# Optimization experiments

Measured on AMD Instinct MI355X. Metric: run time of the kernel, lower is better.

The kernel has to match this reference:

```python
import jax, jax.numpy as jnp
import numpy as np

NUM_EMBEDDINGS = 8192
EMBEDDING_DIM = 256
COMMITMENT_COST = 0.25


def setup_inputs() -> dict:
    key = jax.random.key(0)
    k1, k2 = jax.random.split(key)
    x = jax.random.normal(k1, (8, 4096, EMBEDDING_DIM), dtype=jnp.float32)
    # torch init: uniform(-1/K, 1/K)
    codebook = jax.random.uniform(
        k2, (NUM_EMBEDDINGS, EMBEDDING_DIM), dtype=jnp.float32,
        minval=-1.0 / NUM_EMBEDDINGS, maxval=1.0 / NUM_EMBEDDINGS)
    return {"x": x, "codebook": codebook}


def reference(x, codebook):
    D = codebook.shape[1]
    K = codebook.shape[0]
    flat_x = x.reshape(-1, D)                      # [N, D]
    distances = (jnp.sum(flat_x * flat_x, axis=1, keepdims=True)
                 + jnp.sum(codebook * codebook, axis=1)
                 - 2.0 * jnp.matmul(flat_x, codebook.T))
    encoding_indices = jnp.argmin(distances, axis=1)  # [N]
    # direct gather instead of one-hot matmul (same math)
    quantized = codebook[encoding_indices].reshape(x.shape)

    sg = jax.lax.stop_gradient
    e_latent_loss = jnp.mean((sg(quantized) - x) ** 2)
    q_latent_loss = jnp.mean((quantized - sg(x)) ** 2)
    loss = q_latent_loss + COMMITMENT_COST * e_latent_loss

    quantized_st = x + sg(quantized - x)

    # avg one-hot probs via counts
    counts = jnp.bincount(encoding_indices, length=K)
    avg_probs = counts.astype(x.dtype) / encoding_indices.shape[0]
    perplexity = jnp.exp(-jnp.sum(avg_probs * jnp.log(avg_probs + 1e-10)))
    return quantized_st, loss, perplexity
```

## Files before the change

kernel.cpp:

```cpp
#include <hip/hip_runtime.h>
#include <cfloat>
#include <math.h>

#define NUM_EMB 8192
#define DIM 256
#define NROWS 32768
#define NSPLIT 4
#define CHUNKS 32

typedef float f32x4 __attribute__((ext_vector_type(4)));
typedef int   i32x4 __attribute__((ext_vector_type(4)));
typedef int   i32x8 __attribute__((ext_vector_type(8)));

#define GL2LDS(g, l) __builtin_amdgcn_global_load_lds( \
    (const __attribute__((address_space(1))) void*)(g), \
    (__attribute__((address_space(3))) void*)(l), 16, 0, 0)

#define MFMA(A, B, C) __builtin_amdgcn_mfma_scale_f32_16x16x128_f8f6f4( \
    (A), (B), (C), 0, 0, 0, 127, 0, 127)

__global__ __launch_bounds__(256) void vq_prep(const float* __restrict__ x,
                                               unsigned char* __restrict__ xq,
                                               const float* __restrict__ cb,
                                               unsigned char* __restrict__ cbq,
                                               float* __restrict__ cbn,
                                               unsigned int* __restrict__ counts) {
    int b = blockIdx.x;
    if (b < 4096) {
        int i = b * 256 + threadIdx.x;
        float4 v0 = ((const float4*)x)[2 * i];
        float4 v1 = ((const float4*)x)[2 * i + 1];
        int p0 = __builtin_amdgcn_cvt_pk_fp8_f32(-v0.x, -v0.y, 0, false);
        p0     = __builtin_amdgcn_cvt_pk_fp8_f32(-v0.z, -v0.w, p0, true);
        int p1 = __builtin_amdgcn_cvt_pk_fp8_f32(-v1.x, -v1.y, 0, false);
        p1     = __builtin_amdgcn_cvt_pk_fp8_f32(-v1.z, -v1.w, p1, true);
        ((int2*)xq)[i] = make_int2(p0, p1);
    } else if (b < 6144) {
        int row  = (b - 4096) * 4 + (threadIdx.x >> 6);
        int lane = threadIdx.x & 63;
        float4 v = ((const float4*)(cb + (size_t)row * DIM))[lane];
        int p = __builtin_amdgcn_cvt_pk_fp8_f32(v.x * 8192.f, v.y * 8192.f, 0, false);
        p     = __builtin_amdgcn_cvt_pk_fp8_f32(v.z * 8192.f, v.w * 8192.f, p, true);
        ((int*)cbq)[row * 64 + lane] = p;
        float s = v.x * v.x + v.y * v.y + v.z * v.z + v.w * v.w;
        #pragma unroll
        for (int off = 32; off > 0; off >>= 1) s += __shfl_down(s, off, 64);
        if (lane == 0) cbn[row] = 4096.f * s + 256.f;
    } else {
        counts[(b - 6144) * 256 + threadIdx.x] = 0u;
    }
}

__global__ __launch_bounds__(256, 4) void vq_argmin_mfma(
        const unsigned char* __restrict__ xq,
        const unsigned char* __restrict__ cbq,
        const float* __restrict__ cbn,
        unsigned long long* __restrict__ partial) {
    __shared__ __align__(16) unsigned char Bs[2][16384];
    __shared__ unsigned long long redk[2][64];

    const int tid = threadIdx.x;
    const int lane = tid & 63;
    const int w = tid >> 6;
    const int wm = w >> 1, wn = w & 1;
    const int l15 = lane & 15, q = lane >> 4;
    const int ns = blockIdx.x & (NSPLIT - 1);
    const int by = blockIdx.x >> 2;
    const int m0 = by * 64;
    const int nbase = ns * (NUM_EMB / NSPLIT);

    i32x8 afr00, afr01, afr10, afr11;
    {
        const unsigned char* p = xq + (size_t)(m0 + wm * 32 + l15) * 256 + q * 32;
        i32x4 lo, hi;
        lo = *(const i32x4*)(p);                  hi = *(const i32x4*)(p + 16);
        afr00 = __builtin_shufflevector(lo, hi, 0, 1, 2, 3, 4, 5, 6, 7);
        lo = *(const i32x4*)(p + 16 * 256);       hi = *(const i32x4*)(p + 16 * 256 + 16);
        afr01 = __builtin_shufflevector(lo, hi, 0, 1, 2, 3, 4, 5, 6, 7);
        lo = *(const i32x4*)(p + 128);            hi = *(const i32x4*)(p + 128 + 16);
        afr10 = __builtin_shufflevector(lo, hi, 0, 1, 2, 3, 4, 5, 6, 7);
        lo = *(const i32x4*)(p + 16 * 256 + 128); hi = *(const i32x4*)(p + 16 * 256 + 128 + 16);
        afr11 = __builtin_shufflevector(lo, hi, 0, 1, 2, 3, 4, 5, 6, 7);
    }

    const int row0 = wn * 32 + l15;
    const int sw = row0 & 7;
    const int vA = row0 * 256 + (((2 * q) ^ sw) * 16);
    const int vB = row0 * 256 + (((2 * q + 1) ^ sw) * 16);

    const unsigned int colb0 = (unsigned)(wn * 32 + l15);
    const unsigned int colb1 = colb0 + 16;

    unsigned int runk[2][4];
    #pragma unroll
    for (int i = 0; i < 2; i++)
        #pragma unroll
        for (int r = 0; r < 4; r++) runk[i][r] = 0xFFFFFFFFu;

    const int sr = lane >> 4;
    const int sv = lane & 15;
    const int kcs = sv >> 3, blk = sv & 7;
    const unsigned char* gs[4];
    int sg[4];
    #pragma unroll
    for (int t = 0; t < 4; t++) {
        int s = t * 4 + w;
        int r = s * 4 + sr;
        gs[t] = cbq + (size_t)(nbase + r) * 256 + (size_t)(kcs * 128 + ((blk ^ (r & 7)) * 16));
        sg[t] = s * 1024;
    }

    #pragma unroll
    for (int t = 0; t < 4; t++) GL2LDS(gs[t], (char*)&Bs[0][0] + sg[t]);
    #pragma unroll
    for (int t = 0; t < 4; t++) gs[t] += 16384;
    const float* bnp = cbn + nbase;
    float bn0 = bnp[colb0];
    float bn1 = bnp[colb1];
    __syncthreads();

#define BLOAD(CUR, OFF) ({ \
    i32x4 lo_ = *(const i32x4*)(&Bs[CUR][0] + vA + (OFF)); \
    i32x4 hi_ = *(const i32x4*)(&Bs[CUR][0] + vB + (OFF)); \
    __builtin_shufflevector(lo_, hi_, 0, 1, 2, 3, 4, 5, 6, 7); })

#define CHUNK_BODY(CHV, CUR, NXT, LAST) do { \
    float nbn0 = bnp[64 + (int)colb0]; \
    float nbn1 = bnp[64 + (int)colb1]; \
    if (!(LAST)) { \
        GL2LDS(gs[0], (char*)&Bs[NXT][0] + sg[0]); \
        GL2LDS(gs[1], (char*)&Bs[NXT][0] + sg[1]); \
        GL2LDS(gs[2], (char*)&Bs[NXT][0] + sg[2]); \
        GL2LDS(gs[3], (char*)&Bs[NXT][0] + sg[3]); \
    } \
    gs[0] += 16384; gs[1] += 16384; gs[2] += 16384; gs[3] += 16384; \
    f32x4 ci0; ci0[0] = bn0; ci0[1] = bn0; ci0[2] = bn0; ci0[3] = bn0; \
    f32x4 ci1; ci1[0] = bn1; ci1[1] = bn1; ci1[2] = bn1; ci1[3] = bn1; \
    i32x8 b_ = BLOAD(CUR, 0); \
    f32x4 a00 = MFMA(afr00, b_, ci0); \
    f32x4 a10 = MFMA(afr01, b_, ci0); \
    b_ = BLOAD(CUR, 128); \
    a00 = MFMA(afr10, b_, a00); \
    a10 = MFMA(afr11, b_, a10); \
    b_ = BLOAD(CUR, 4096); \
    f32x4 a01 = MFMA(afr00, b_, ci1); \
    f32x4 a11 = MFMA(afr01, b_, ci1); \
    b_ = BLOAD(CUR, 4224); \
    a01 = MFMA(afr10, b_, a01); \
    a11 = MFMA(afr11, b_, a11); \
    unsigned int chb = ((unsigned)(CHV)) << 6; \
    unsigned int cj0 = chb | colb0, cj1 = chb | colb1; \
    _Pragma("unroll") \
    for (int r = 0; r < 4; r++) { \
        unsigned int k00 = (__float_as_uint(a00[r]) & 0xFFFFF800u) | cj0; \
        unsigned int k01 = (__float_as_uint(a01[r]) & 0xFFFFF800u) | cj1; \
        runk[0][r] = min(min(k00, k01), runk[0][r]); \
        unsigned int k10 = (__float_as_uint(a10[r]) & 0xFFFFF800u) | cj0; \
        unsigned int k11 = (__float_as_uint(a11[r]) & 0xFFFFF800u) | cj1; \
        runk[1][r] = min(min(k10, k11), runk[1][r]); \
    } \
    bn0 = nbn0; bn1 = nbn1; bnp += 64; \
    __syncthreads(); \
} while (0)

    #pragma unroll 1
    for (int ch = 0; ch < CHUNKS; ch += 2) {
        CHUNK_BODY(ch,     0, 1, false);
        CHUNK_BODY(ch + 1, 1, 0, (ch + 1) == CHUNKS - 1);
    }

    #pragma unroll
    for (int i = 0; i < 2; i++) {
        #pragma unroll
        for (int r = 0; r < 4; r++) {
            unsigned int rk = runk[i][r];
            unsigned int gcol = (unsigned)nbase + (rk & 0x7FFu);
            unsigned long long key =
                ((unsigned long long)(rk & 0xFFFFF800u) << 32) | gcol;
            #pragma unroll
            for (int off = 8; off >= 1; off >>= 1) {
                unsigned long long o = __shfl_xor(key, off, 16);
                if (o < key) key = o;
            }
            if (l15 == 0) redk[wn][wm * 32 + i * 16 + q * 4 + r] = key;
        }
    }
    __syncthreads();
    if (tid < 64) {
        unsigned long long k0 = redk[0][tid], k1 = redk[1][tid];
        partial[(size_t)ns * NROWS + m0 + tid] = k0 < k1 ? k0 : k1;
    }
}

__global__ __launch_bounds__(256) void vq_out(const float* __restrict__ x,
                                              const float* __restrict__ cb,
                                              const unsigned long long* __restrict__ partial,
                                              float* __restrict__ out,
                                              unsigned int* __restrict__ counts,
                                              double* __restrict__ loss_part) {
    __shared__ float wred[4];
    int wv   = threadIdx.x >> 6;
    int row  = blockIdx.x * 4 + wv;
    int lane = threadIdx.x & 63;
    unsigned long long k = 0xFFFFFFFFFFFFFFFFull;
    #pragma unroll
    for (int t = 0; t < NSPLIT; t++) {
        unsigned long long v = partial[(size_t)t * NROWS + row];
        if (v < k) k = v;
    }
    int id = (int)(unsigned int)(k & 0xffffffffu);
    float4 qv = ((const float4*)(cb + (size_t)id * DIM))[lane];
    float4 xv = ((const float4*)(x + (size_t)row * DIM))[lane];
    float dx = qv.x - xv.x, dy = qv.y - xv.y, dz = qv.z - xv.z, dw = qv.w - xv.w;
    float4 o;
    o.x = xv.x + dx; o.y = xv.y + dy; o.z = xv.z + dz; o.w = xv.w + dw;
    ((float4*)(out + (size_t)row * DIM))[lane] = o;
    float s = dx * dx + dy * dy + dz * dz + dw * dw;
    #pragma unroll
    for (int o2 = 32; o2 > 0; o2 >>= 1) s += __shfl_down(s, o2, 64);
    if (lane == 0) {
        wred[wv] = s;
        atomicAdd(&counts[id], 1u);
    }
    __syncthreads();
    if (threadIdx.x == 0) {
        loss_part[blockIdx.x] =
            (double)wred[0] + (double)wred[1] + (double)wred[2] + (double)wred[3];
    }
}

__global__ __launch_bounds__(256) void vq_fin(const unsigned int* __restrict__ counts,
                                              const double* __restrict__ loss_part,
                                              float* __restrict__ out_tail) {
    __shared__ double sh[256];
    __shared__ double sl[256];
    int tid = threadIdx.x;
    double h = 0.0;
    for (int k = tid; k < NUM_EMB; k += 256) {
        float p = (float)counts[k] / 32768.0f;
        h += (double)p * log((double)p + 1e-10);
    }
    double ls = 0.0;
    for (int b = tid; b < NROWS / 4; b += 256) ls += loss_part[b];
    sh[tid] = h;
    sl[tid] = ls;
    __syncthreads();
    for (int o = 128; o > 0; o >>= 1) {
        if (tid < o) { sh[tid] += sh[tid + o]; sl[tid] += sl[tid + o]; }
        __syncthreads();
    }
    if (tid == 0) {
        double mean = sl[0] / (double)((size_t)NROWS * DIM);
        out_tail[0] = (float)(1.25 * mean);
        out_tail[1] = (float)exp(-sh[0]);
    }
}

extern "C" void kernel_launch(void* const* d_in, const int* in_sizes, int n_in,
                              void* d_out, int out_size, void* d_ws, size_t ws_size,
                              hipStream_t stream) {
    const float* x  = (const float*)d_in[0];
    const float* cb = (const float*)d_in[1];
    char* ws = (char*)d_ws;
    unsigned int* counts   = (unsigned int*)(ws + 256);
    float* cbn             = (float*)(ws + 33024);
    unsigned char* xq      = (unsigned char*)(ws + 65792);
    unsigned char* cbq     = (unsigned char*)(ws + 65792 + 8388608);
    unsigned long long* pp = (unsigned long long*)(ws + 65792 + 8388608 + 2097152);
    double* loss_part      = (double*)(ws + 65792 + 8388608 + 2097152 + 16777216);
    float* out = (float*)d_out;

    vq_prep       <<<6176, 256, 0, stream>>>(x, xq, cb, cbq, cbn, counts);
    vq_argmin_mfma<<<512 * NSPLIT, 256, 0, stream>>>(xq, cbq, cbn, pp);
    vq_out        <<<8192, 256, 0, stream>>>(x, cb, pp, out, counts, loss_part);
    vq_fin        <<<1, 256, 0, stream>>>(counts, loss_part, out + (size_t)NROWS * DIM);
}
```

Baseline: 200.7 us.

## Coarsen prep/out kernels, batch LDS B loads, and use fast log in finalize

The x-quantization blocks in vq_prep now handle two 256-element slices each, and vq_out blocks handle four rows per wave, cutting the launch grids and the number of loss partials. Inside the argmin MFMA loop, all four B fragments are loaded from LDS before the eight MFMAs, with a sched_barrier after the async global-to-LDS loads, so LDS latency can overlap. The finalize kernel uses __logf in float instead of double log. These changes trade lower block-launch overhead and better latency hiding for higher register pressure and slightly lower entropy precision.

```diff
diff --git a/kernel.cpp b/kernel.cpp
--- a/kernel.cpp
+++ b/kernel.cpp
@@ -26,17 +26,20 @@
                                                float* __restrict__ cbn,
                                                unsigned int* __restrict__ counts) {
     int b = blockIdx.x;
-    if (b < 4096) {
-        int i = b * 256 + threadIdx.x;
-        float4 v0 = ((const float4*)x)[2 * i];
-        float4 v1 = ((const float4*)x)[2 * i + 1];
-        int p0 = __builtin_amdgcn_cvt_pk_fp8_f32(-v0.x, -v0.y, 0, false);
-        p0     = __builtin_amdgcn_cvt_pk_fp8_f32(-v0.z, -v0.w, p0, true);
-        int p1 = __builtin_amdgcn_cvt_pk_fp8_f32(-v1.x, -v1.y, 0, false);
-        p1     = __builtin_amdgcn_cvt_pk_fp8_f32(-v1.z, -v1.w, p1, true);
-        ((int2*)xq)[i] = make_int2(p0, p1);
-    } else if (b < 6144) {
-        int row  = (b - 4096) * 4 + (threadIdx.x >> 6);
+    if (b < 2048) {
+        #pragma unroll
+        for (int j = 0; j < 2; j++) {
+            int i = b * 512 + j * 256 + threadIdx.x;
+            float4 v0 = ((const float4*)x)[2 * i];
+            float4 v1 = ((const float4*)x)[2 * i + 1];
+            int p0 = __builtin_amdgcn_cvt_pk_fp8_f32(-v0.x, -v0.y, 0, false);
+            p0     = __builtin_amdgcn_cvt_pk_fp8_f32(-v0.z, -v0.w, p0, true);
+            int p1 = __builtin_amdgcn_cvt_pk_fp8_f32(-v1.x, -v1.y, 0, false);
+            p1     = __builtin_amdgcn_cvt_pk_fp8_f32(-v1.z, -v1.w, p1, true);
+            ((int2*)xq)[i] = make_int2(p0, p1);
+        }
+    } else if (b < 4096) {
+        int row  = (b - 2048) * 4 + (threadIdx.x >> 6);
         int lane = threadIdx.x & 63;
         float4 v = ((const float4*)(cb + (size_t)row * DIM))[lane];
         int p = __builtin_amdgcn_cvt_pk_fp8_f32(v.x * 8192.f, v.y * 8192.f, 0, false);
@@ -47,7 +50,7 @@
         for (int off = 32; off > 0; off >>= 1) s += __shfl_down(s, off, 64);
         if (lane == 0) cbn[row] = 4096.f * s + 256.f;
     } else {
-        counts[(b - 6144) * 256 + threadIdx.x] = 0u;
+        counts[(b - 4096) * 256 + threadIdx.x] = 0u;
     }
 }
 
@@ -132,22 +135,23 @@
         GL2LDS(gs[1], (char*)&Bs[NXT][0] + sg[1]); \
         GL2LDS(gs[2], (char*)&Bs[NXT][0] + sg[2]); \
         GL2LDS(gs[3], (char*)&Bs[NXT][0] + sg[3]); \
+        __builtin_amdgcn_sched_barrier(0); \
     } \
     gs[0] += 16384; gs[1] += 16384; gs[2] += 16384; gs[3] += 16384; \
+    i32x8 b0 = BLOAD(CUR, 0); \
+    i32x8 b1 = BLOAD(CUR, 128); \
+    i32x8 b2 = BLOAD(CUR, 4096); \
+    i32x8 b3 = BLOAD(CUR, 4224); \
     f32x4 ci0; ci0[0] = bn0; ci0[1] = bn0; ci0[2] = bn0; ci0[3] = bn0; \
     f32x4 ci1; ci1[0] = bn1; ci1[1] = bn1; ci1[2] = bn1; ci1[3] = bn1; \
-    i32x8 b_ = BLOAD(CUR, 0); \
-    f32x4 a00 = MFMA(afr00, b_, ci0); \
-    f32x4 a10 = MFMA(afr01, b_, ci0); \
-    b_ = BLOAD(CUR, 128); \
-    a00 = MFMA(afr10, b_, a00); \
-    a10 = MFMA(afr11, b_, a10); \
-    b_ = BLOAD(CUR, 4096); \
-    f32x4 a01 = MFMA(afr00, b_, ci1); \
-    f32x4 a11 = MFMA(afr01, b_, ci1); \
-    b_ = BLOAD(CUR, 4224); \
-    a01 = MFMA(afr10, b_, a01); \
-    a11 = MFMA(afr11, b_, a11); \
+    f32x4 a00 = MFMA(afr00, b0, ci0); \
+    f32x4 a10 = MFMA(afr01, b0, ci0); \
+    f32x4 a01 = MFMA(afr00, b2, ci1); \
+    f32x4 a11 = MFMA(afr01, b2, ci1); \
+    a00 = MFMA(afr10, b1, a00); \
+    a10 = MFMA(afr11, b1, a10); \
+    a01 = MFMA(afr10, b3, a01); \
+    a11 = MFMA(afr11, b3, a11); \
     unsigned int chb = ((unsigned)(CHV)) << 6; \
     unsigned int cj0 = chb | colb0, cj1 = chb | colb1; \
     _Pragma("unroll") \
@@ -200,28 +204,33 @@
                                               double* __restrict__ loss_part) {
     __shared__ float wred[4];
     int wv   = threadIdx.x >> 6;
-    int row  = blockIdx.x * 4 + wv;
     int lane = threadIdx.x & 63;
-    unsigned long long k = 0xFFFFFFFFFFFFFFFFull;
-    #pragma unroll
-    for (int t = 0; t < NSPLIT; t++) {
-        unsigned long long v = partial[(size_t)t * NROWS + row];
-        if (v < k) k = v;
-    }
-    int id = (int)(unsigned int)(k & 0xffffffffu);
-    float4 qv = ((const float4*)(cb + (size_t)id * DIM))[lane];
-    float4 xv = ((const float4*)(x + (size_t)row * DIM))[lane];
-    float dx = qv.x - xv.x, dy = qv.y - xv.y, dz = qv.z - xv.z, dw = qv.w - xv.w;
-    float4 o;
-    o.x = xv.x + dx; o.y = xv.y + dy; o.z = xv.z + dz; o.w = xv.w + dw;
-    ((float4*)(out + (size_t)row * DIM))[lane] = o;
-    float s = dx * dx + dy * dy + dz * dz + dw * dw;
-    #pragma unroll
-    for (int o2 = 32; o2 > 0; o2 >>= 1) s += __shfl_down(s, o2, 64);
-    if (lane == 0) {
-        wred[wv] = s;
-        atomicAdd(&counts[id], 1u);
-    }
+    float wsum = 0.f;
+    #pragma unroll
+    for (int rr = 0; rr < 4; rr++) {
+        int row = blockIdx.x * 16 + wv * 4 + rr;
+        unsigned long long k = 0xFFFFFFFFFFFFFFFFull;
+        #pragma unroll
+        for (int t = 0; t < NSPLIT; t++) {
+            unsigned long long v = partial[(size_t)t * NROWS + row];
+            if (v < k) k = v;
+        }
+        int id = (int)(unsigned int)(k & 0xffffffffu);
+        float4 qv = ((const float4*)(cb + (size_t)id * DIM))[lane];
+        float4 xv = ((const float4*)(x + (size_t)row * DIM))[lane];
+        float dx = qv.x - xv.x, dy = qv.y - xv.y, dz = qv.z - xv.z, dw = qv.w - xv.w;
+        float4 o;
+        o.x = xv.x + dx; o.y = xv.y + dy; o.z = xv.z + dz; o.w = xv.w + dw;
+        ((float4*)(out + (size_t)row * DIM))[lane] = o;
+        float s = dx * dx + dy * dy + dz * dz + dw * dw;
+        #pragma unroll
+        for (int o2 = 32; o2 > 0; o2 >>= 1) s += __shfl_down(s, o2, 64);
+        if (lane == 0) {
+            wsum += s;
+            atomicAdd(&counts[id], 1u);
+        }
+    }
+    if (lane == 0) wred[wv] = wsum;
     __syncthreads();
     if (threadIdx.x == 0) {
         loss_part[blockIdx.x] =
@@ -237,11 +246,11 @@
     int tid = threadIdx.x;
     double h = 0.0;
     for (int k = tid; k < NUM_EMB; k += 256) {
-        float p = (float)counts[k] / 32768.0f;
-        h += (double)p * log((double)p + 1e-10);
+        float p = (float)counts[k] * (1.0f / 32768.0f);
+        h += (double)(p * __logf(p + 1e-10f));
     }
     double ls = 0.0;
-    for (int b = tid; b < NROWS / 4; b += 256) ls += loss_part[b];
+    for (int b = tid; b < NROWS / 16; b += 256) ls += loss_part[b];
     sh[tid] = h;
     sl[tid] = ls;
     __syncthreads();
@@ -270,8 +279,8 @@
     double* loss_part      = (double*)(ws + 65792 + 8388608 + 2097152 + 16777216);
     float* out = (float*)d_out;
 
-    vq_prep       <<<6176, 256, 0, stream>>>(x, xq, cb, cbq, cbn, counts);
+    vq_prep       <<<4128, 256, 0, stream>>>(x, xq, cb, cbq, cbn, counts);
     vq_argmin_mfma<<<512 * NSPLIT, 256, 0, stream>>>(xq, cbq, cbn, pp);
-    vq_out        <<<8192, 256, 0, stream>>>(x, cb, pp, out, counts, loss_part);
+    vq_out        <<<2048, 256, 0, stream>>>(x, cb, pp, out, counts, loss_part);
     vq_fin        <<<1, 256, 0, stream>>>(counts, loss_part, out + (size_t)NROWS * DIM);
 }
```

After: 192.4 us. 1.04x faster.
